# Performance work log

Hardware: AMD Instinct MI355X
Metric: run time of the kernel (lower is better)

## Reference

```python
import jax, jax.numpy as jnp
import numpy as np

D = 1024        # embedding_dim
N = 200000      # number of train embeddings
C = 50          # n_concepts
B = 4096        # batch size
NUM_CLASSES = 4
TOPK = 50


def setup_inputs() -> dict:
    key = jax.random.key(0)
    k1, k2, k3, k4, k5 = jax.random.split(key, 5)
    return {
        "concept": jax.random.normal(k1, (D, C), dtype=jnp.float32),
        "train_embeddings": jax.random.normal(k2, (D, N), dtype=jnp.float32),
        "train_embedding": jax.random.normal(k3, (B, D), dtype=jnp.float32),
        "hx_weight": jax.random.normal(k4, (NUM_CLASSES, D), dtype=jnp.float32) * 0.02,
        "hx_bias": jax.random.normal(k5, (NUM_CLASSES,), dtype=jnp.float32) * 0.02,
        "topk": TOPK,
    }


def reference(concept, train_embeddings, train_embedding, hx_weight, hx_bias, topk):
    n_concepts = concept.shape[1]
    k = int(topk)

    # projection of inputs onto concept subspace: P = C (C^T C)^{-1} C^T
    gram = concept.T @ concept                      # (C, C)
    proj_matrix = concept @ jnp.linalg.inv(gram) @ concept.T   # (D, D)
    proj = proj_matrix @ train_embedding.T          # (D, B)
    y_pred = proj.T @ hx_weight.T + hx_bias         # (B, num_classes)
    orig_pred = train_embedding @ hx_weight.T + hx_bias

    # batched KNN: squared euclidean distance of every concept to every train embedding
    # (sqrt is monotone, ordering identical to torch.norm-based distances)
    te_sq = jnp.sum(train_embeddings * train_embeddings, axis=0)   # (N,)
    c_sq = jnp.sum(concept * concept, axis=0)                      # (C,)
    dots = concept.T @ train_embeddings                            # (C, N)
    dist2 = c_sq[:, None] + te_sq[None, :] - 2.0 * dots            # (C, N)
    _, knn_idx = jax.lax.top_k(-dist2, k)                          # (C, k) smallest distances

    # gather neighbor activations: (D, C, k)
    knn_act = jnp.take(train_embeddings, knn_idx.reshape(-1), axis=1).reshape(
        train_embeddings.shape[0], n_concepts, k)

    # L_sparse_1 = mean_c [ sum_{d,k} concept[d,c]*knn[d,c,k] / k ]
    L_sparse_1 = jnp.einsum("dc,dck->", concept, knn_act) / (k * n_concepts)

    eye = jnp.eye(n_concepts, dtype=concept.dtype)
    mask = 1.0 - eye
    L_sparse_2 = jnp.mean(gram * mask)
    norm_metrics = jnp.mean(gram * eye)
    similarity_penalty = jnp.mean(jnp.abs(gram - eye))

    return (orig_pred, y_pred, L_sparse_1, L_sparse_2, norm_metrics, similarity_penalty)
```

## Files before the change

kernel.cpp:

```cpp
#include <hip/hip_runtime.h>
#include <hip/hip_bf16.h>
#include <stdint.h>

#define D 1024
#define N 200000
#define C 50
#define B 4096
#define CLS 4
#define KParts 16
#define CAP 4096
#define BN 256
#define NBLK 782
#define NSLOT (NBLK * 8)
#define BLROW 260

typedef __attribute__((ext_vector_type(8))) short short8;
typedef __attribute__((ext_vector_type(4))) float f32x4;

static const size_t OFF_U     = 0;
static const size_t OFF_TESQ  = (size_t)C * N;
static const size_t OFF_GPART = OFF_TESQ + N;
static const size_t OFF_WPART = OFF_GPART + KParts * 2500;
static const size_t OFF_ABF   = ((OFF_WPART + KParts * 200 + 3) / 4) * 4;
static const size_t OFF_RANGE = OFF_ABF + 32768;
static const size_t OFF_SUMS  = OFF_RANGE + 2 * NSLOT;
static const size_t OFF_CNT   = OFF_SUMS + C;
static const size_t OFF_W8    = ((OFF_CNT + 1 + 3) / 4) * 4;

__device__ __forceinline__ unsigned mapf(float v) {
    unsigned u = __float_as_uint(v);
    return (u & 0x80000000u) ? ~u : (u | 0x80000000u);
}
__device__ __forceinline__ float unmapf(unsigned u) {
    unsigned b = (u & 0x80000000u) ? (u ^ 0x80000000u) : ~u;
    return __uint_as_float(b);
}
__device__ __forceinline__ unsigned keyu(float dot, float tesq) {
    return mapf(fmaf(-2.0f, dot, tesq));
}
__device__ __forceinline__ unsigned short f2bf(float f) {
    unsigned u = __float_as_uint(f);
    u += 0x7FFFu + ((u >> 16) & 1u);
    return (unsigned short)(u >> 16);
}

#define TILE_BARRIER() do {                                   \
    asm volatile("s_waitcnt lgkmcnt(0)" ::: "memory");        \
    __builtin_amdgcn_s_barrier();                             \
    asm volatile("" ::: "memory");                            \
} while (0)

__global__ __launch_bounds__(256) void kprep(
    const float* __restrict__ concept, const float* __restrict__ hxw,
    float* __restrict__ ws)
{
    int t = threadIdx.x;

    if (blockIdx.x < KParts) {
        __shared__ __align__(16) float ct[64 * 50];
        __shared__ float hs[4 * 64];
        int bid = blockIdx.x;
        int d0 = bid * 64;

        for (int i = t; i < 64 * 50; i += 256) ct[i] = concept[d0 * 50 + i];
        {
            int j = t >> 6, dd = t & 63;
            hs[t] = hxw[j * D + d0 + dd];
        }
        __syncthreads();

        float* gp = ws + OFF_GPART + (size_t)bid * 2500;
        for (int p = t; p < 2500; p += 256) {
            int i = p / 50, j = p - i * 50;
            float acc = 0.f;
            #pragma unroll 8
            for (int dd = 0; dd < 64; ++dd)
                acc = fmaf(ct[dd * 50 + i], ct[dd * 50 + j], acc);
            gp[p] = acc;
        }
        float* wp = ws + OFF_WPART + (size_t)bid * 200;
        if (t < 200) {
            int j = t / 50, c = t - j * 50;
            float acc = 0.f;
            #pragma unroll 8
            for (int dd = 0; dd < 64; ++dd)
                acc = fmaf(hs[j * 64 + dd], ct[dd * 50 + c], acc);
            wp[t] = acc;
        }
        return;
    }

    unsigned short* ap = (unsigned short*)(ws + OFF_ABF);
    for (int idx = t; idx < 8192; idx += 256) {
        int ks = idx >> 8;
        int g  = (idx >> 6) & 3;
        int m  = idx & 63;
        unsigned short v[8];
        #pragma unroll
        for (int j = 0; j < 8; ++j) {
            int k = ks * 32 + g * 8 + j;
            v[j] = (m < 50) ? f2bf(concept[k * 50 + m]) : (unsigned short)0;
        }
        uint4 pk;
        pk.x = (unsigned)v[0] | ((unsigned)v[1] << 16);
        pk.y = (unsigned)v[2] | ((unsigned)v[3] << 16);
        pk.z = (unsigned)v[4] | ((unsigned)v[5] << 16);
        pk.w = (unsigned)v[6] | ((unsigned)v[7] << 16);
        *(uint4*)(ap + (size_t)idx * 8) = pk;
    }
}

__global__ __launch_bounds__(512, 4) void kgemm(
    const float* __restrict__ concept, const float* __restrict__ te,
    const float* __restrict__ hxw, float* __restrict__ ws,
    float* __restrict__ out)
{
    __shared__ __align__(16) unsigned char smem[42496];

    int t = threadIdx.x;
    int l = t & 63, w = t >> 6;

    if (blockIdx.x == NBLK) {
        float* gsh  = (float*)smem;
        float* Asv  = (float*)(smem + 10000);
        float* colp = (float*)(smem + 21200);
        float* part = (float*)(smem + 21408);

        if (t == 0) ((unsigned*)(ws + OFF_CNT))[0] = 0u;

        float s_all = 0.f, s_tr = 0.f, s_abs = 0.f;
        for (int p = t; p < 2500; p += 512) {
            float g = 0.f;
            #pragma unroll
            for (int b = 0; b < KParts; ++b)
                g += ws[OFF_GPART + (size_t)b * 2500 + p];
            gsh[p] = g;
            int i = p / 50, jj = p - i * 50;
            float e = (i == jj) ? 1.0f : 0.0f;
            s_all += g;
            if (i == jj) s_tr += g;
            s_abs += fabsf(g - e);
        }
        #pragma unroll
        for (int off = 32; off > 0; off >>= 1) {
            s_all += __shfl_down(s_all, off, 64);
            s_tr  += __shfl_down(s_tr,  off, 64);
            s_abs += __shfl_down(s_abs, off, 64);
        }
        if (l == 0) { part[0 * 8 + w] = s_all; part[1 * 8 + w] = s_tr; part[2 * 8 + w] = s_abs; }
        __syncthreads();
        if (t == 0) {
            float a = 0.f, tr = 0.f, ab = 0.f;
            for (int i = 0; i < 8; ++i) {
                a += part[0 * 8 + i]; tr += part[1 * 8 + i]; ab += part[2 * 8 + i];
            }
            out[32769] = (a - tr) / 2500.0f;
            out[32770] = tr / 2500.0f;
            out[32771] = ab / 2500.0f;
        }

        for (int p = t; p < 50 * 56; p += 512) {
            int r = p / 56, col = p - r * 56;
            float v = 0.f;
            if (col < 50) v = gsh[r * 50 + col];
            else if (col < 54) {
                float ww = 0.f;
                #pragma unroll
                for (int b = 0; b < KParts; ++b)
                    ww += ws[OFF_WPART + (size_t)b * 200 + (col - 50) * 50 + r];
                v = ww;
            }
            Asv[p] = v;
        }
        __syncthreads();

        for (int pc = 0; pc < C; ++pc) {
            if (t < C) colp[t] = Asv[t * 56 + pc];
            __syncthreads();
            float pinv = 1.0f / colp[pc];
            if (t < 56) Asv[pc * 56 + t] *= pinv;
            __syncthreads();
            for (int p = t; p < 50 * 56; p += 512) {
                int r = p / 56, col = p - r * 56;
                if (r != pc) Asv[p] = fmaf(-colp[r], Asv[pc * 56 + col], Asv[p]);
            }
            __syncthreads();
        }

        for (int d = t; d < D; d += 512) {
            float wy0 = 0.f, wy1 = 0.f, wy2 = 0.f, wy3 = 0.f;
            for (int c = 0; c < C; ++c) {
                float cv = concept[d * 50 + c];
                wy0 = fmaf(cv, Asv[c * 56 + 50], wy0);
                wy1 = fmaf(cv, Asv[c * 56 + 51], wy1);
                wy2 = fmaf(cv, Asv[c * 56 + 52], wy2);
                wy3 = fmaf(cv, Asv[c * 56 + 53], wy3);
            }
            float4 lo, hi;
            lo.x = hxw[0 * D + d]; lo.y = hxw[1 * D + d];
            lo.z = hxw[2 * D + d]; lo.w = hxw[3 * D + d];
            hi.x = wy0; hi.y = wy1; hi.z = wy2; hi.w = wy3;
            *(float4*)(ws + OFF_W8 + (size_t)d * 8)     = lo;
            *(float4*)(ws + OFF_W8 + (size_t)d * 8 + 4) = hi;
        }
        return;
    }

    unsigned* Blb = (unsigned*)smem;
    float* tsp = (float*)(smem + 33280);
    float* tsf = (float*)(smem + 33280 + 8192);

    int nbase = blockIdx.x * BN;
    int nq = t & 63, rp = w;
    int ncol0 = nbase + nq * 4;
    bool colv = (ncol0 < N);

    f32x4 accf[2][4];
    #pragma unroll
    for (int mf = 0; mf < 2; ++mf)
        #pragma unroll
        for (int nf = 0; nf < 4; ++nf)
            accf[mf][nf] = (f32x4)(0.0f);
    float ts0 = 0.f, ts1 = 0.f, ts2 = 0.f, ts3 = 0.f;

    const unsigned short* ap = (const unsigned short*)(ws + OFF_ABF);
    int g = l >> 4;
    int mhalf = w >> 2;
    int nnb = (w & 3) * 64 + (l & 15);

    auto ldtile = [&](int ks, float4* xr) {
        #pragma unroll
        for (int pi = 0; pi < 2; ++pi) {
            int pair = rp + pi * 8;
            int k0 = ks * 32 + pair * 2;
            if (colv) {
                xr[2 * pi]     = *(const float4*)(te + (size_t)k0 * N + ncol0);
                xr[2 * pi + 1] = *(const float4*)(te + (size_t)(k0 + 1) * N + ncol0);
            } else {
                xr[2 * pi]     = make_float4(0.f, 0.f, 0.f, 0.f);
                xr[2 * pi + 1] = make_float4(0.f, 0.f, 0.f, 0.f);
            }
        }
    };

    auto cvt_write = [&](int buf, float4* xr) {
        #pragma unroll
        for (int pi = 0; pi < 2; ++pi) {
            int pair = rp + pi * 8;
            float4 xa = xr[2 * pi], xb = xr[2 * pi + 1];
            union { __hip_bfloat162 h; unsigned u; } p0, p1, p2, p3;
            p0.h = __float22bfloat162_rn(make_float2(xa.x, xb.x));
            p1.h = __float22bfloat162_rn(make_float2(xa.y, xb.y));
            p2.h = __float22bfloat162_rn(make_float2(xa.z, xb.z));
            p3.h = __float22bfloat162_rn(make_float2(xa.w, xb.w));
            float fa0 = __uint_as_float(p0.u << 16), fb0 = __uint_as_float(p0.u & 0xFFFF0000u);
            float fa1 = __uint_as_float(p1.u << 16), fb1 = __uint_as_float(p1.u & 0xFFFF0000u);
            float fa2 = __uint_as_float(p2.u << 16), fb2 = __uint_as_float(p2.u & 0xFFFF0000u);
            float fa3 = __uint_as_float(p3.u << 16), fb3 = __uint_as_float(p3.u & 0xFFFF0000u);
            ts0 = fmaf(fa0, fa0, fmaf(fb0, fb0, ts0));
            ts1 = fmaf(fa1, fa1, fmaf(fb1, fb1, ts1));
            ts2 = fmaf(fa2, fa2, fmaf(fb2, fb2, ts2));
            ts3 = fmaf(fa3, fa3, fmaf(fb3, fb3, ts3));
            uint4 pk;
            pk.x = p0.u; pk.y = p1.u; pk.z = p2.u; pk.w = p3.u;
            *(uint4*)(&Blb[buf * (16 * BLROW) + pair * BLROW + nq * 4]) = pk;
        }
    };

    auto body = [&](int ks, float4* rload, float4* rcons) {
        if (ks < 30) ldtile(ks + 2, rload);

        short8 af0 = *(const short8*)(ap + ((size_t)(ks * 4 + g) * 64 + mhalf * 32 + 0 * 16 + (l & 15)) * 8);
        short8 af1 = *(const short8*)(ap + ((size_t)(ks * 4 + g) * 64 + mhalf * 32 + 1 * 16 + (l & 15)) * 8);

        const unsigned* Bc = Blb + (ks & 1) * (16 * BLROW);
        #pragma unroll
        for (int nf = 0; nf < 4; ++nf) {
            int nn = nnb + nf * 16;
            union { unsigned u[4]; short8 s; } bu;
            bu.u[0] = Bc[(g * 4 + 0) * BLROW + nn];
            bu.u[1] = Bc[(g * 4 + 1) * BLROW + nn];
            bu.u[2] = Bc[(g * 4 + 2) * BLROW + nn];
            bu.u[3] = Bc[(g * 4 + 3) * BLROW + nn];
            accf[0][nf] = __builtin_amdgcn_mfma_f32_16x16x32_bf16(af0, bu.s, accf[0][nf], 0, 0, 0);
            accf[1][nf] = __builtin_amdgcn_mfma_f32_16x16x32_bf16(af1, bu.s, accf[1][nf], 0, 0, 0);
        }

        if (ks < 31) cvt_write((ks + 1) & 1, rcons);
    };

    float4 r0[4], r1[4];
    ldtile(0, r0);
    ldtile(1, r1);
    cvt_write(0, r0);

    #pragma unroll 1
    for (int ks = 0; ks < 32; ks += 2) {
        TILE_BARRIER();
        body(ks, r0, r1);
        TILE_BARRIER();
        body(ks + 1, r1, r0);
    }

    __syncthreads();
    tsp[rp * 256 + nq * 4 + 0] = ts0;
    tsp[rp * 256 + nq * 4 + 1] = ts1;
    tsp[rp * 256 + nq * 4 + 2] = ts2;
    tsp[rp * 256 + nq * 4 + 3] = ts3;
    __syncthreads();
    if (t < 64) {
        float4 s = make_float4(0.f, 0.f, 0.f, 0.f);
        #pragma unroll
        for (int r = 0; r < 8; ++r) {
            float4 v = *(const float4*)(&tsp[r * 256 + t * 4]);
            s.x += v.x; s.y += v.y; s.z += v.z; s.w += v.w;
        }
        *(float4*)(&tsf[t * 4]) = s;
        if (nbase + t * 4 < N)
            *(float4*)(ws + OFF_TESQ + nbase + t * 4) = s;
    }
    __syncthreads();

    unsigned* uws = (unsigned*)ws;
    unsigned kmin = 0xFFFFFFFFu, kmax = 0u;
    #pragma unroll
    for (int mf = 0; mf < 2; ++mf) {
        #pragma unroll
        for (int nf = 0; nf < 4; ++nf) {
            int nloc = nnb + nf * 16;
            int nabs = nbase + nloc;
            #pragma unroll
            for (int r = 0; r < 4; ++r) {
                int c = mhalf * 32 + mf * 16 + (l >> 4) * 4 + r;
                if (c < 50 && nabs < N) {
                    unsigned u = keyu(accf[mf][nf][r], tsf[nloc]);
                    uws[(size_t)c * N + nabs] = u;
                    kmin = min(kmin, u);
                    kmax = max(kmax, u);
                }
            }
        }
    }
    #pragma unroll
    for (int off = 32; off > 0; off >>= 1) {
        kmin = min(kmin, (unsigned)__shfl_down((int)kmin, off, 64));
        kmax = max(kmax, (unsigned)__shfl_down((int)kmax, off, 64));
    }
    if (l == 0) {
        int slot = blockIdx.x * 8 + w;
        ((unsigned*)(ws + OFF_RANGE))[2 * slot]     = kmin;
        ((unsigned*)(ws + OFF_RANGE))[2 * slot + 1] = kmax;
    }
}

__global__ __launch_bounds__(256) void kpred(
    const float* __restrict__ X, const float* __restrict__ hxb,
    const float* __restrict__ ws, float* __restrict__ out)
{
    int t = threadIdx.x;
    int lane = t & 63, w = t >> 6;
    int r = blockIdx.x * 4 + w;
    const float* xr = X + (size_t)r * D;
    const float* w8 = ws + OFF_W8;

    float acc[8];
    #pragma unroll
    for (int j = 0; j < 8; ++j) acc[j] = 0.f;
    #pragma unroll
    for (int i = 0; i < 16; ++i) {
        int d = i * 64 + lane;
        float x = xr[d];
        float4 lo = *(const float4*)(w8 + (size_t)d * 8);
        float4 hi = *(const float4*)(w8 + (size_t)d * 8 + 4);
        acc[0] = fmaf(x, lo.x, acc[0]);
        acc[1] = fmaf(x, lo.y, acc[1]);
        acc[2] = fmaf(x, lo.z, acc[2]);
        acc[3] = fmaf(x, lo.w, acc[3]);
        acc[4] = fmaf(x, hi.x, acc[4]);
        acc[5] = fmaf(x, hi.y, acc[5]);
        acc[6] = fmaf(x, hi.z, acc[6]);
        acc[7] = fmaf(x, hi.w, acc[7]);
    }
    #pragma unroll
    for (int j = 0; j < 8; ++j) {
        float v = acc[j];
        #pragma unroll
        for (int off = 32; off > 0; off >>= 1) v += __shfl_down(v, off, 64);
        if (lane == 0) {
            float b = hxb[j & 3];
            if (j < 4) out[(size_t)r * CLS + j] = v + b;
            else       out[16384 + (size_t)r * CLS + (j - 4)] = v + b;
        }
    }
}

__global__ __launch_bounds__(1024) void k4_select(
    const float* __restrict__ ws, float* __restrict__ wsw,
    float* __restrict__ out, const int* __restrict__ topk)
{
    int c = blockIdx.x, t = threadIdx.x;
    int lane = t & 63, wid = t >> 6;
    const unsigned* uarr = (const unsigned*)ws + (size_t)c * N;
    const float* tesq = ws + OFF_TESQ;

    __shared__ unsigned hist[4096];
    __shared__ unsigned wsum[16], woff[16];
    __shared__ unsigned wmn[16], wmx[16];
    __shared__ unsigned sh_ulo, sh_uhi;
    __shared__ unsigned sh_bin; __shared__ int sh_rem;
    __shared__ int cnt;
    __shared__ unsigned cand_u[CAP];
    __shared__ int      cand_i[CAP];
    __shared__ float fred[16];

    {
        const unsigned* rg = (const unsigned*)(ws + OFF_RANGE);
        unsigned mn = 0xFFFFFFFFu, mx = 0u;
        for (int i = t; i < NSLOT; i += 1024) {
            mn = min(mn, rg[2 * i]);
            mx = max(mx, rg[2 * i + 1]);
        }
        #pragma unroll
        for (int off = 32; off > 0; off >>= 1) {
            mn = min(mn, (unsigned)__shfl_down((int)mn, off, 64));
            mx = max(mx, (unsigned)__shfl_down((int)mx, off, 64));
        }
        if (lane == 0) { wmn[wid] = mn; wmx[wid] = mx; }
        __syncthreads();
        if (t == 0) {
            unsigned m0 = 0xFFFFFFFFu, m1 = 0u;
            for (int w = 0; w < 16; ++w) { m0 = min(m0, wmn[w]); m1 = max(m1, wmx[w]); }
            sh_ulo = m0; sh_uhi = m1;
        }
        __syncthreads();
    }
    unsigned ubase = sh_ulo;
    unsigned ulo = sh_ulo, uhi = sh_uhi;
    int rem = *topk;
    unsigned long long width = (unsigned long long)(uhi - ulo) + 1ull;

    for (int i = t; i < 4096; i += 1024) hist[i] = 0u;
    __syncthreads();
    for (int n = t; n < N; n += 1024) {
        unsigned u = uarr[n];
        unsigned bin = (unsigned)(((unsigned long long)(u - ubase) * 4096ull) / width);
        atomicAdd(&hist[bin], 1u);
    }
    __syncthreads();
    {
        unsigned b0 = (unsigned)t * 4u;
        unsigned h0 = hist[b0], h1 = hist[b0 + 1], h2 = hist[b0 + 2], h3 = hist[b0 + 3];
        unsigned s4 = h0 + h1 + h2 + h3;
        unsigned x = s4;
        #pragma unroll
        for (int off = 1; off < 64; off <<= 1) {
            unsigned y = (unsigned)__shfl_up((int)x, off, 64);
            if (lane >= off) x += y;
        }
        if (lane == 63) wsum[wid] = x;
        __syncthreads();
        if (t == 0) {
            unsigned run = 0;
            for (int w = 0; w < 16; ++w) { woff[w] = run; run += wsum[w]; }
        }
        __syncthreads();
        unsigned cumBefore = woff[wid] + x - s4;
        unsigned remu = (unsigned)rem;
        if (cumBefore < remu && remu <= cumBefore + s4) {
            unsigned cum = cumBefore, bin = b0, r2 = 1;
            unsigned hh[4] = {h0, h1, h2, h3};
            #pragma unroll
            for (int j = 0; j < 4; ++j) {
                if (cum + hh[j] >= remu) { bin = b0 + j; r2 = remu - cum; break; }
                cum += hh[j];
            }
            sh_bin = bin; sh_rem = (int)r2;
        }
        __syncthreads();
        unsigned b = sh_bin;
        rem = sh_rem;
        ulo = ubase + (unsigned)(((unsigned long long)b * width + 4095ull) / 4096ull);
        uhi = ubase + (unsigned)((((unsigned long long)(b + 1) * width + 4095ull) / 4096ull) - 1ull);
        __syncthreads();
    }

    if (t == 0) cnt = 0;
    __syncthreads();
    float lsum = 0.f;
    for (int n = t; n < N; n += 1024) {
        unsigned u = uarr[n];
        if (u < ulo) {
            lsum += 0.5f * (tesq[n] - unmapf(u));
        } else if (u <= uhi) {
            int s = atomicAdd(&cnt, 1);
            if (s < CAP) { cand_u[s] = u; cand_i[s] = n; }
        }
    }
    __syncthreads();
    int cc = cnt < CAP ? cnt : CAP;
    for (int ci = t; ci < cc; ci += 1024) {
        unsigned ui = cand_u[ci]; int ii = cand_i[ci];
        int rank = 0;
        for (int j = 0; j < cc; ++j) {
            unsigned uj = cand_u[j];
            rank += (uj < ui || (uj == ui && cand_i[j] < ii)) ? 1 : 0;
        }
        if (rank < rem) lsum += 0.5f * (tesq[ii] - unmapf(ui));
    }
    #pragma unroll
    for (int off = 32; off > 0; off >>= 1) lsum += __shfl_down(lsum, off, 64);
    if (lane == 0) fred[wid] = lsum;
    __syncthreads();
    if (t == 0) {
        float tot = 0.f;
        for (int w = 0; w < 16; ++w) tot += fred[w];
        wsw[OFF_SUMS + c] = tot;
        __threadfence();
        unsigned done = atomicAdd((unsigned*)(wsw + OFF_CNT), 1u);
        if (done == C - 1) {
            float s = 0.f;
            for (int i = 0; i < C; ++i) s += atomicAdd(&wsw[OFF_SUMS + i], 0.0f);
            out[32768] = s / (float)((*topk) * C);
        }
    }
}

extern "C" void kernel_launch(void* const* d_in, const int* in_sizes, int n_in,
                              void* d_out, int out_size, void* d_ws, size_t ws_size,
                              hipStream_t stream) {
    (void)in_sizes; (void)n_in; (void)out_size; (void)ws_size;
    const float* concept = (const float*)d_in[0];
    const float* te      = (const float*)d_in[1];
    const float* X       = (const float*)d_in[2];
    const float* hxw     = (const float*)d_in[3];
    const float* hxb     = (const float*)d_in[4];
    const int*   topk    = (const int*)d_in[5];
    float* out = (float*)d_out;
    float* ws  = (float*)d_ws;

    kprep<<<dim3(KParts + 1), dim3(256), 0, stream>>>(concept, hxw, ws);
    kgemm<<<dim3(NBLK + 1), dim3(512), 0, stream>>>(concept, te, hxw, ws, out);
    kpred<<<dim3(B / 4), dim3(256), 0, stream>>>(X, hxb, ws, out);
    k4_select<<<dim3(C), dim3(1024), 0, stream>>>(ws, ws, out, topk);
}
```

Before: 508.2 us.

## Pre-convert train embeddings to packed bf16 tiles in a separate pass

Adds a transpose/convert pass to the prep kernel. It reads the fp32 train embeddings once and writes bf16 row-pair packed tiles laid out per GEMM block into workspace. The GEMM kernel then loads these contiguous packed tiles instead of strided fp32 rows and skips in-loop conversion. This adds a full extra write and read of roughly half the embedding size (about 400MB in bf16), so total memory traffic likely rises for a bandwidth-bound workload.

```diff
diff --git a/kernel.cpp b/kernel.cpp
--- a/kernel.cpp
+++ b/kernel.cpp
@@ -13,6 +13,8 @@
 #define NBLK 782
 #define NSLOT (NBLK * 8)
 #define BLROW 260
+#define TWORK 784
+#define NTASK (512 * 49)
 
 typedef __attribute__((ext_vector_type(8))) short short8;
 typedef __attribute__((ext_vector_type(4))) float f32x4;
@@ -26,6 +28,7 @@
 static const size_t OFF_SUMS  = OFF_RANGE + 2 * NSLOT;
 static const size_t OFF_CNT   = OFF_SUMS + C;
 static const size_t OFF_W8    = ((OFF_CNT + 1 + 3) / 4) * 4;
+static const size_t OFF_PK    = OFF_W8 + (size_t)D * 8;
 
 __device__ __forceinline__ unsigned mapf(float v) {
     unsigned u = __float_as_uint(v);
@@ -50,11 +53,12 @@
     asm volatile("" ::: "memory");                            \
 } while (0)
 
-__global__ __launch_bounds__(256) void kprep(
-    const float* __restrict__ concept, const float* __restrict__ hxw,
-    float* __restrict__ ws)
+__global__ __launch_bounds__(256) void ktrans(
+    const float* __restrict__ concept, const float* __restrict__ te,
+    const float* __restrict__ hxw, float* __restrict__ ws)
 {
     int t = threadIdx.x;
+    int l = t & 63, w = t >> 6;
 
     if (blockIdx.x < KParts) {
         __shared__ __align__(16) float ct[64 * 50];
@@ -90,30 +94,64 @@
         return;
     }
 
-    unsigned short* ap = (unsigned short*)(ws + OFF_ABF);
-    for (int idx = t; idx < 8192; idx += 256) {
-        int ks = idx >> 8;
-        int g  = (idx >> 6) & 3;
-        int m  = idx & 63;
-        unsigned short v[8];
-        #pragma unroll
-        for (int j = 0; j < 8; ++j) {
-            int k = ks * 32 + g * 8 + j;
-            v[j] = (m < 50) ? f2bf(concept[k * 50 + m]) : (unsigned short)0;
-        }
-        uint4 pk;
-        pk.x = (unsigned)v[0] | ((unsigned)v[1] << 16);
-        pk.y = (unsigned)v[2] | ((unsigned)v[3] << 16);
-        pk.z = (unsigned)v[4] | ((unsigned)v[5] << 16);
-        pk.w = (unsigned)v[6] | ((unsigned)v[7] << 16);
-        *(uint4*)(ap + (size_t)idx * 8) = pk;
+    if (blockIdx.x == KParts) {
+        unsigned short* ap = (unsigned short*)(ws + OFF_ABF);
+        for (int idx = t; idx < 8192; idx += 256) {
+            int ks = idx >> 8;
+            int g  = (idx >> 6) & 3;
+            int m  = idx & 63;
+            unsigned short v[8];
+            #pragma unroll
+            for (int j = 0; j < 8; ++j) {
+                int k = ks * 32 + g * 8 + j;
+                v[j] = (m < 50) ? f2bf(concept[k * 50 + m]) : (unsigned short)0;
+            }
+            uint4 pk;
+            pk.x = (unsigned)v[0] | ((unsigned)v[1] << 16);
+            pk.y = (unsigned)v[2] | ((unsigned)v[3] << 16);
+            pk.z = (unsigned)v[4] | ((unsigned)v[5] << 16);
+            pk.w = (unsigned)v[6] | ((unsigned)v[7] << 16);
+            *(uint4*)(ap + (size_t)idx * 8) = pk;
+        }
+        return;
+    }
+
+    unsigned* pkb = (unsigned*)(ws + OFF_PK);
+    int gw = (blockIdx.x - (KParts + 1)) * 4 + w;
+    for (int task = gw; task < NTASK; task += TWORK * 4) {
+        int j = task / 512;
+        int p = task - j * 512;
+        const float* r0 = te + (size_t)(2 * p) * N;
+        const float* r1 = te + (size_t)(2 * p + 1) * N;
+        #pragma unroll 4
+        for (int q = 0; q < 16; ++q) {
+            int c = j * 4096 + q * 256 + l * 4;
+            float4 x0, x1;
+            if (c < N) {
+                x0 = *(const float4*)(r0 + c);
+                x1 = *(const float4*)(r1 + c);
+            } else {
+                x0 = make_float4(0.f, 0.f, 0.f, 0.f);
+                x1 = make_float4(0.f, 0.f, 0.f, 0.f);
+            }
+            union { __hip_bfloat162 h; unsigned u; } p0, p1, p2, p3;
+            p0.h = __float22bfloat162_rn(make_float2(x0.x, x1.x));
+            p1.h = __float22bfloat162_rn(make_float2(x0.y, x1.y));
+            p2.h = __float22bfloat162_rn(make_float2(x0.z, x1.z));
+            p3.h = __float22bfloat162_rn(make_float2(x0.w, x1.w));
+            int nb = j * 16 + q;
+            if (nb < NBLK) {
+                uint4 pk;
+                pk.x = p0.u; pk.y = p1.u; pk.z = p2.u; pk.w = p3.u;
+                *(uint4*)(pkb + (size_t)nb * 131072 + (size_t)p * 256 + l * 4) = pk;
+            }
+        }
     }
 }
 
 __global__ __launch_bounds__(512, 4) void kgemm(
-    const float* __restrict__ concept, const float* __restrict__ te,
-    const float* __restrict__ hxw, float* __restrict__ ws,
-    float* __restrict__ out)
+    const float* __restrict__ concept, const float* __restrict__ hxw,
+    float* __restrict__ ws, float* __restrict__ out)
 {
     __shared__ __align__(16) unsigned char smem[42496];
 
@@ -212,8 +250,7 @@
 
     int nbase = blockIdx.x * BN;
     int nq = t & 63, rp = w;
-    int ncol0 = nbase + nq * 4;
-    bool colv = (ncol0 < N);
+    bool colv = true; (void)colv;
 
     f32x4 accf[2][4];
     #pragma unroll
@@ -224,50 +261,37 @@
     float ts0 = 0.f, ts1 = 0.f, ts2 = 0.f, ts3 = 0.f;
 
     const unsigned short* ap = (const unsigned short*)(ws + OFF_ABF);
+    const unsigned* pkt = (const unsigned*)(ws + OFF_PK) + (size_t)blockIdx.x * 131072;
     int g = l >> 4;
     int mhalf = w >> 2;
     int nnb = (w & 3) * 64 + (l & 15);
 
-    auto ldtile = [&](int ks, float4* xr) {
+    auto ldtile = [&](int ks, uint4* xr) {
         #pragma unroll
         for (int pi = 0; pi < 2; ++pi) {
             int pair = rp + pi * 8;
-            int k0 = ks * 32 + pair * 2;
-            if (colv) {
-                xr[2 * pi]     = *(const float4*)(te + (size_t)k0 * N + ncol0);
-                xr[2 * pi + 1] = *(const float4*)(te + (size_t)(k0 + 1) * N + ncol0);
-            } else {
-                xr[2 * pi]     = make_float4(0.f, 0.f, 0.f, 0.f);
-                xr[2 * pi + 1] = make_float4(0.f, 0.f, 0.f, 0.f);
-            }
+            xr[pi] = *(const uint4*)(pkt + (size_t)(ks * 16 + pair) * 256 + nq * 4);
         }
     };
 
-    auto cvt_write = [&](int buf, float4* xr) {
+    auto stage_write = [&](int buf, uint4* xr) {
         #pragma unroll
         for (int pi = 0; pi < 2; ++pi) {
             int pair = rp + pi * 8;
-            float4 xa = xr[2 * pi], xb = xr[2 * pi + 1];
-            union { __hip_bfloat162 h; unsigned u; } p0, p1, p2, p3;
-            p0.h = __float22bfloat162_rn(make_float2(xa.x, xb.x));
-            p1.h = __float22bfloat162_rn(make_float2(xa.y, xb.y));
-            p2.h = __float22bfloat162_rn(make_float2(xa.z, xb.z));
-            p3.h = __float22bfloat162_rn(make_float2(xa.w, xb.w));
-            float fa0 = __uint_as_float(p0.u << 16), fb0 = __uint_as_float(p0.u & 0xFFFF0000u);
-            float fa1 = __uint_as_float(p1.u << 16), fb1 = __uint_as_float(p1.u & 0xFFFF0000u);
-            float fa2 = __uint_as_float(p2.u << 16), fb2 = __uint_as_float(p2.u & 0xFFFF0000u);
-            float fa3 = __uint_as_float(p3.u << 16), fb3 = __uint_as_float(p3.u & 0xFFFF0000u);
+            uint4 v = xr[pi];
+            float fa0 = __uint_as_float(v.x << 16), fb0 = __uint_as_float(v.x & 0xFFFF0000u);
+            float fa1 = __uint_as_float(v.y << 16), fb1 = __uint_as_float(v.y & 0xFFFF0000u);
+            float fa2 = __uint_as_float(v.z << 16), fb2 = __uint_as_float(v.z & 0xFFFF0000u);
+            float fa3 = __uint_as_float(v.w << 16), fb3 = __uint_as_float(v.w & 0xFFFF0000u);
             ts0 = fmaf(fa0, fa0, fmaf(fb0, fb0, ts0));
             ts1 = fmaf(fa1, fa1, fmaf(fb1, fb1, ts1));
             ts2 = fmaf(fa2, fa2, fmaf(fb2, fb2, ts2));
             ts3 = fmaf(fa3, fa3, fmaf(fb3, fb3, ts3));
-            uint4 pk;
-            pk.x = p0.u; pk.y = p1.u; pk.z = p2.u; pk.w = p3.u;
-            *(uint4*)(&Blb[buf * (16 * BLROW) + pair * BLROW + nq * 4]) = pk;
+            *(uint4*)(&Blb[buf * (16 * BLROW) + pair * BLROW + nq * 4]) = v;
         }
     };
 
-    auto body = [&](int ks, float4* rload, float4* rcons) {
+    auto body = [&](int ks, uint4* rload, uint4* rcons) {
         if (ks < 30) ldtile(ks + 2, rload);
 
         short8 af0 = *(const short8*)(ap + ((size_t)(ks * 4 + g) * 64 + mhalf * 32 + 0 * 16 + (l & 15)) * 8);
@@ -286,13 +310,13 @@
             accf[1][nf] = __builtin_amdgcn_mfma_f32_16x16x32_bf16(af1, bu.s, accf[1][nf], 0, 0, 0);
         }
 
-        if (ks < 31) cvt_write((ks + 1) & 1, rcons);
+        if (ks < 31) stage_write((ks + 1) & 1, rcons);
     };
 
-    float4 r0[4], r1[4];
+    uint4 r0[2], r1[2];
     ldtile(0, r0);
     ldtile(1, r1);
-    cvt_write(0, r0);
+    stage_write(0, r0);
 
     #pragma unroll 1
     for (int ks = 0; ks < 32; ks += 2) {
@@ -538,8 +562,8 @@
     float* out = (float*)d_out;
     float* ws  = (float*)d_ws;
 
-    kprep<<<dim3(KParts + 1), dim3(256), 0, stream>>>(concept, hxw, ws);
-    kgemm<<<dim3(NBLK + 1), dim3(512), 0, stream>>>(concept, te, hxw, ws, out);
+    ktrans<<<dim3(KParts + 1 + TWORK), dim3(256), 0, stream>>>(concept, te, hxw, ws);
+    kgemm<<<dim3(NBLK + 1), dim3(512), 0, stream>>>(concept, hxw, ws, out);
     kpred<<<dim3(B / 4), dim3(256), 0, stream>>>(X, hxb, ws, out);
     k4_select<<<dim3(C), dim3(1024), 0, stream>>>(ws, ws, out, topk);
 }
```

Measured after the change: 669.2 us. +31.7%, slower.
